# Performance work log

Measured on AMD Instinct MI355X. Metric: run time of the kernel, lower is better.

## Reference

```python
import jax, jax.numpy as jnp
import numpy as np

B, S, D, INNER = 4, 2048, 1024, 64  # batch, seq_len, input_size, cfg.inner_dim


def setup_inputs() -> dict:
    key = jax.random.key(0)
    ks = jax.random.split(key, 5)
    sequence_outputs = jax.random.normal(ks[0], (B, S, D), jnp.float32)
    W = jax.random.normal(ks[1], (INNER * 4, D), jnp.float32) * 0.02
    b = jnp.zeros((INNER * 4,), jnp.float32)
    similarity = jax.random.normal(ks[2], (B, S, S, 1), jnp.float32)
    input_labels = jax.random.randint(ks[3], (B, S, S), 0, 2)
    masks = jax.random.randint(ks[4], (B, S, S), 0, 2)
    return {"sequence_outputs": sequence_outputs, "W": W, "b": b,
            "similarity": similarity, "input_labels": input_labels, "masks": masks}


def _sincos(seq_len, dim):
    # RoPE with base 15 (pos_type=1 in the original code)
    pos = jnp.arange(seq_len, dtype=jnp.float32)[:, None]          # (S,1)
    inv = 15.0 ** (-2.0 * jnp.arange(dim // 2, dtype=jnp.float32) / dim)
    ang = pos * inv                                                # (S, dim/2)
    # interleaved [sin0,cos0,sin1,cos1,...] -> repeat_interleave(2) of odd/even slices
    sin = jnp.repeat(jnp.sin(ang), 2, axis=-1)                     # (S, dim)
    cos = jnp.repeat(jnp.cos(ang), 2, axis=-1)                     # (S, dim)
    return sin[None, :, None, :], cos[None, :, None, :]            # (1,S,1,dim)


def _rope(x, sin, cos):
    # x: (B,S,H,dim); rotate-half with interleaved pairs
    x2 = jnp.stack([-x[..., 1::2], x[..., ::2]], axis=-1).reshape(x.shape)
    return x * cos + x2 * sin


def reference(sequence_outputs, W, b, similarity, input_labels, masks):
    # dense: (B,S,D) -> (B,S,4*INNER); split into 2 chunks of 2*INNER, stacked on dim -2
    out = sequence_outputs @ W.T + b                               # (B,S,4I)
    out = out.reshape(B, S, 2, 2 * INNER)                          # (B,S,h=2,2I)
    qw, kw = out[..., :INNER], out[..., INNER:]                    # (B,S,2,I) each

    sin, cos = _sincos(S, INNER)
    qw = _rope(qw, sin, cos)
    kw = _rope(kw, sin, cos)

    pred_logits = jnp.einsum('bmhd,bnhd->bmnh', qw, kw) * similarity  # (B,S,S,2)

    # masked cross-entropy (CrossEntropyLoss with unit class weights, mean reduction)
    logp = jax.nn.log_softmax(pred_logits.reshape(-1, 2), axis=-1)
    lab = input_labels.reshape(-1)
    nll = -jnp.take_along_axis(logp, lab[:, None], axis=1)[:, 0]
    m = (masks.reshape(-1) == 1).astype(pred_logits.dtype)
    loss = jnp.sum(nll * m) / jnp.sum(m)
    return (loss, pred_logits)
```

## Files before the change

### kernel.cpp

```cpp
#include <hip/hip_runtime.h>
#include <hip/hip_bf16.h>
#include <math.h>

#define B_     4
#define S_     2048
#define D_     1024
#define INNER_ 64
#define M_     (B_ * S_)

typedef __attribute__((ext_vector_type(8))) short short8v;
typedef __attribute__((ext_vector_type(4))) float f32x4;

__device__ __forceinline__ unsigned short f32_to_bf16_rne(float f) {
    unsigned u = __float_as_uint(f);
    unsigned r = (u + 0x7FFFu + ((u >> 16) & 1u)) >> 16;
    return (unsigned short)r;
}
__device__ __forceinline__ float bf16_to_f32(unsigned short h) {
    return __uint_as_float((unsigned)h << 16);
}

__global__ __launch_bounds__(256)
void gemm1_rope_kernel(const float* __restrict__ seq, const float* __restrict__ W,
                       const float* __restrict__ bias,
                       unsigned short* __restrict__ qhl, unsigned short* __restrict__ khl) {
    const int bm = blockIdx.x;
    const int bn = blockIdx.y;
    __shared__ float As[16][65];
    __shared__ float Bs[16][65];
    __shared__ float s_inv[32];

    const int tid = threadIdx.x;
    if (tid < 32) s_inv[tid] = powf(15.0f, -(float)tid / 32.0f);

    const int tr = tid >> 4;
    const int tc = tid & 15;
    const int row0 = bm * 64, col0 = bn * 64;

    const int lr = tid >> 2;
    const int lc = (tid & 3) * 4;

    float acc[4][4] = {};

    for (int k0 = 0; k0 < D_; k0 += 16) {
        float4 av = *reinterpret_cast<const float4*>(&seq[(size_t)(row0 + lr) * D_ + k0 + lc]);
        float4 bv = *reinterpret_cast<const float4*>(&W  [(size_t)(col0 + lr) * D_ + k0 + lc]);
        As[lc + 0][lr] = av.x; As[lc + 1][lr] = av.y; As[lc + 2][lr] = av.z; As[lc + 3][lr] = av.w;
        Bs[lc + 0][lr] = bv.x; Bs[lc + 1][lr] = bv.y; Bs[lc + 2][lr] = bv.z; Bs[lc + 3][lr] = bv.w;
        __syncthreads();
#pragma unroll
        for (int kk = 0; kk < 16; ++kk) {
            float a[4], b[4];
#pragma unroll
            for (int i = 0; i < 4; ++i) a[i] = As[kk][tr * 4 + i];
#pragma unroll
            for (int j = 0; j < 4; ++j) b[j] = Bs[kk][tc * 4 + j];
#pragma unroll
            for (int i = 0; i < 4; ++i)
#pragma unroll
                for (int j = 0; j < 4; ++j)
                    acc[i][j] = fmaf(a[i], b[j], acc[i][j]);
        }
        __syncthreads();
    }

#pragma unroll
    for (int i = 0; i < 4; ++i) {
        const int m = row0 + tr * 4 + i;
        const int s = m & (S_ - 1);
#pragma unroll
        for (int jj = 0; jj < 4; jj += 2) {
            const int j = col0 + tc * 4 + jj;
            const float x0 = acc[i][jj]     + bias[j];
            const float x1 = acc[i][jj + 1] + bias[j + 1];
            const int h = j >> 7;
            const int c = j & 127;
            const int d = c & 63;
            const float inv = s_inv[d >> 1];
            const float ang = (float)s * inv;
            float sn, cs;
            __sincosf(ang, &sn, &cs);
            const float r0 = x0 * cs - x1 * sn;
            const float r1 = x1 * cs + x0 * sn;
            unsigned short* dst = (c < 64) ? qhl : khl;
            const unsigned short h0 = f32_to_bf16_rne(r0);
            const unsigned short h1 = f32_to_bf16_rne(r1);
            const unsigned short l0 = f32_to_bf16_rne(r0 - bf16_to_f32(h0));
            const unsigned short l1 = f32_to_bf16_rne(r1 - bf16_to_f32(h1));
            const size_t base = (size_t)m * 256 + (size_t)h * 128 + d;
            *reinterpret_cast<ushort2*>(&dst[base])      = make_ushort2(h0, h1);
            *reinterpret_cast<ushort2*>(&dst[base + 64]) = make_ushort2(l0, l1);
        }
    }
}

__global__ __launch_bounds__(256)
void qk_loss_kernel(const unsigned short* __restrict__ qhl,
                    const unsigned short* __restrict__ khl,
                    const float* __restrict__ sim, const int* __restrict__ labels,
                    const int* __restrict__ masks, float* __restrict__ logits,
                    double* __restrict__ accum) {
    const int bidx = blockIdx.x;
    const int bb = bidx >> 10;
    const int mt = (bidx >> 5) & 31;
    const int nt = bidx & 31;

    __shared__ __align__(16) unsigned short Ks[64][264];

    const int tid  = threadIdx.x;
    const int w    = tid >> 6;
    const int lane = tid & 63;
    const int lrow = lane & 15;
    const int lkg  = lane >> 4;

    {
        const unsigned short* kbase = khl + ((size_t)bb * S_ + (size_t)nt * 64) * 256;
#pragma unroll
        for (int it = 0; it < 8; ++it) {
            const int f = it * 256 + tid;
            const int r = f >> 5;
            const int ch = f & 31;
            *reinterpret_cast<uint4*>(reinterpret_cast<char*>(&Ks[0][0]) + r * 528 + ch * 16) =
                *reinterpret_cast<const uint4*>(kbase + (size_t)r * 256 + ch * 8);
        }
    }

    short8v qf[2][2][2];
    {
        const int mrow = mt * 64 + w * 16 + lrow;
        const unsigned short* qrow = qhl + ((size_t)bb * S_ + mrow) * 256;
#pragma unroll
        for (int h = 0; h < 2; ++h)
#pragma unroll
            for (int p = 0; p < 2; ++p)
#pragma unroll
                for (int s = 0; s < 2; ++s)
                    qf[h][p][s] = *reinterpret_cast<const short8v*>(
                        qrow + h * 128 + p * 64 + s * 32 + lkg * 8);
    }
    __syncthreads();

    f32x4 acc[2][4];
#pragma unroll
    for (int h = 0; h < 2; ++h)
#pragma unroll
        for (int cg = 0; cg < 4; ++cg)
            acc[h][cg] = (f32x4){0.f, 0.f, 0.f, 0.f};

#pragma unroll
    for (int h = 0; h < 2; ++h) {
#pragma unroll
        for (int cg = 0; cg < 4; ++cg) {
#pragma unroll
            for (int s = 0; s < 2; ++s) {
                const char* krow = reinterpret_cast<const char*>(&Ks[0][0]) +
                                   (cg * 16 + lrow) * 528 +
                                   h * 256 + s * 64 + lkg * 16;
                const short8v kh = *reinterpret_cast<const short8v*>(krow);
                const short8v kl = *reinterpret_cast<const short8v*>(krow + 128);
                acc[h][cg] = __builtin_amdgcn_mfma_f32_16x16x32_bf16(qf[h][0][s], kh, acc[h][cg], 0, 0, 0);
                acc[h][cg] = __builtin_amdgcn_mfma_f32_16x16x32_bf16(qf[h][0][s], kl, acc[h][cg], 0, 0, 0);
                acc[h][cg] = __builtin_amdgcn_mfma_f32_16x16x32_bf16(qf[h][1][s], kh, acc[h][cg], 0, 0, 0);
            }
        }
    }

    float lsum = 0.f, msum = 0.f;
#pragma unroll
    for (int cg = 0; cg < 4; ++cg) {
        const int n = nt * 64 + cg * 16 + lrow;
#pragma unroll
        for (int r = 0; r < 4; ++r) {
            const int m = mt * 64 + w * 16 + lkg * 4 + r;
            const size_t cell = ((size_t)bb * S_ + m) * S_ + n;
            const float sv = sim[cell];
            const float l0 = acc[0][cg][r] * sv;
            const float l1 = acc[1][cg][r] * sv;
            *reinterpret_cast<float2*>(&logits[cell * 2]) = make_float2(l0, l1);
            const int lab = labels[cell];
            const float mk = (masks[cell] == 1) ? 1.0f : 0.0f;
            const float mx = fmaxf(l0, l1);
            const float mn = fminf(l0, l1);
            const float lse = mx + log1pf(expf(mn - mx));
            const float nll = lse - (lab ? l1 : l0);
            lsum += nll * mk;
            msum += mk;
        }
    }

#pragma unroll
    for (int off = 32; off > 0; off >>= 1) {
        lsum += __shfl_down(lsum, off);
        msum += __shfl_down(msum, off);
    }
    __shared__ double wred[8];
    if (lane == 0) {
        wred[w]     = (double)lsum;
        wred[4 + w] = (double)msum;
    }
    __syncthreads();
    if (tid == 0) {
        atomicAdd(&accum[0], wred[0] + wred[1] + wred[2] + wred[3]);
        atomicAdd(&accum[1], wred[4] + wred[5] + wred[6] + wred[7]);
    }
}

__global__ void finalize_kernel(const double* __restrict__ accum, float* __restrict__ out) {
    out[0] = (float)(accum[0] / accum[1]);
}

extern "C" void kernel_launch(void* const* d_in, const int* in_sizes, int n_in,
                              void* d_out, int out_size, void* d_ws, size_t ws_size,
                              hipStream_t stream) {
    const float* seq    = (const float*)d_in[0];
    const float* W      = (const float*)d_in[1];
    const float* bias   = (const float*)d_in[2];
    const float* sim    = (const float*)d_in[3];
    const int*   labels = (const int*)d_in[4];
    const int*   masks  = (const int*)d_in[5];
    float* out = (float*)d_out;

    double* accum = (double*)d_ws;
    unsigned short* qhl = (unsigned short*)((char*)d_ws + 256);
    unsigned short* khl = qhl + (size_t)M_ * 256;

    hipMemsetAsync(d_ws, 0, 16, stream);

    dim3 gA(M_ / 64, 4);
    gemm1_rope_kernel<<<gA, 256, 0, stream>>>(seq, W, bias, qhl, khl);

    qk_loss_kernel<<<4096, 256, 0, stream>>>(qhl, khl, sim, labels, masks,
                                             out + 1, accum);

    finalize_kernel<<<1, 1, 0, stream>>>(accum, out);
}
```

Measured before the change: 498.8 us.

## Move projection GEMM to split-bf16 MFMA and split loss into separate kernel

```diff
diff --git a/kernel.cpp b/kernel.cpp
--- a/kernel.cpp
+++ b/kernel.cpp
@@ -5,7 +5,6 @@
 #define B_     4
 #define S_     2048
 #define D_     1024
-#define INNER_ 64
 #define M_     (B_ * S_)
 
 typedef __attribute__((ext_vector_type(8))) short short8v;
@@ -13,130 +12,148 @@
 
 __device__ __forceinline__ unsigned short f32_to_bf16_rne(float f) {
     unsigned u = __float_as_uint(f);
-    unsigned r = (u + 0x7FFFu + ((u >> 16) & 1u)) >> 16;
-    return (unsigned short)r;
+    return (unsigned short)((u + 0x7FFFu + ((u >> 16) & 1u)) >> 16);
 }
 __device__ __forceinline__ float bf16_to_f32(unsigned short h) {
     return __uint_as_float((unsigned)h << 16);
 }
 
-__global__ __launch_bounds__(256)
-void gemm1_rope_kernel(const float* __restrict__ seq, const float* __restrict__ W,
+__global__ __launch_bounds__(512)
+void gemm1_rope_kernel(const float* __restrict__ seq,
+                       const float* __restrict__ W,
                        const float* __restrict__ bias,
                        unsigned short* __restrict__ qhl, unsigned short* __restrict__ khl) {
     const int bm = blockIdx.x;
-    const int bn = blockIdx.y;
-    __shared__ float As[16][65];
-    __shared__ float Bs[16][65];
+    const int tid = threadIdx.x;
+    const int w = tid >> 6, lane = tid & 63;
+    const int lrow = lane & 15, lkg = lane >> 4;
+    const int wm = (w & 1) * 16;
+    const int jq = w >> 1;
+    const int m0 = bm * 32;
+
+    __shared__ __align__(16) unsigned short Sh[32][40], Sl[32][40];
+    __shared__ __align__(16) unsigned short Wth[256][40], Wtl[256][40];
     __shared__ float s_inv[32];
 
-    const int tid = threadIdx.x;
-    if (tid < 32) s_inv[tid] = powf(15.0f, -(float)tid / 32.0f);
-
-    const int tr = tid >> 4;
-    const int tc = tid & 15;
-    const int row0 = bm * 64, col0 = bn * 64;
-
-    const int lr = tid >> 2;
-    const int lc = (tid & 3) * 4;
-
-    float acc[4][4] = {};
-
-    for (int k0 = 0; k0 < D_; k0 += 16) {
-        float4 av = *reinterpret_cast<const float4*>(&seq[(size_t)(row0 + lr) * D_ + k0 + lc]);
-        float4 bv = *reinterpret_cast<const float4*>(&W  [(size_t)(col0 + lr) * D_ + k0 + lc]);
-        As[lc + 0][lr] = av.x; As[lc + 1][lr] = av.y; As[lc + 2][lr] = av.z; As[lc + 3][lr] = av.w;
-        Bs[lc + 0][lr] = bv.x; Bs[lc + 1][lr] = bv.y; Bs[lc + 2][lr] = bv.z; Bs[lc + 3][lr] = bv.w;
+    if (tid < 32) s_inv[tid] = (float)pow(15.0, -(double)tid / 32.0);
+
+    f32x4 acc[4];
+#pragma unroll
+    for (int i = 0; i < 4; ++i) acc[i] = (f32x4){0.f, 0.f, 0.f, 0.f};
+
+    const int srow = tid >> 3, scol = (tid & 7) * 4;
+
+    for (int k0 = 0; k0 < D_; k0 += 32) {
+        if (tid < 256) {
+            const float4 v = *reinterpret_cast<const float4*>(
+                seq + (size_t)(m0 + srow) * D_ + k0 + scol);
+            const unsigned short h0 = f32_to_bf16_rne(v.x), h1 = f32_to_bf16_rne(v.y),
+                                 h2 = f32_to_bf16_rne(v.z), h3 = f32_to_bf16_rne(v.w);
+            *reinterpret_cast<ushort4*>(&Sh[srow][scol]) = make_ushort4(h0, h1, h2, h3);
+            *reinterpret_cast<ushort4*>(&Sl[srow][scol]) =
+                make_ushort4(f32_to_bf16_rne(v.x - bf16_to_f32(h0)),
+                             f32_to_bf16_rne(v.y - bf16_to_f32(h1)),
+                             f32_to_bf16_rne(v.z - bf16_to_f32(h2)),
+                             f32_to_bf16_rne(v.w - bf16_to_f32(h3)));
+        }
+#pragma unroll
+        for (int p = 0; p < 4; ++p) {
+            const int c = tid + p * 512;
+            const int j = c >> 3;
+            const int kk = (c & 7) * 4;
+            const float4 v = *reinterpret_cast<const float4*>(
+                W + (size_t)j * D_ + k0 + kk);
+            const unsigned short h0 = f32_to_bf16_rne(v.x), h1 = f32_to_bf16_rne(v.y),
+                                 h2 = f32_to_bf16_rne(v.z), h3 = f32_to_bf16_rne(v.w);
+            *reinterpret_cast<ushort4*>(&Wth[j][kk]) = make_ushort4(h0, h1, h2, h3);
+            *reinterpret_cast<ushort4*>(&Wtl[j][kk]) =
+                make_ushort4(f32_to_bf16_rne(v.x - bf16_to_f32(h0)),
+                             f32_to_bf16_rne(v.y - bf16_to_f32(h1)),
+                             f32_to_bf16_rne(v.z - bf16_to_f32(h2)),
+                             f32_to_bf16_rne(v.w - bf16_to_f32(h3)));
+        }
         __syncthreads();
-#pragma unroll
-        for (int kk = 0; kk < 16; ++kk) {
-            float a[4], b[4];
-#pragma unroll
-            for (int i = 0; i < 4; ++i) a[i] = As[kk][tr * 4 + i];
-#pragma unroll
-            for (int j = 0; j < 4; ++j) b[j] = Bs[kk][tc * 4 + j];
-#pragma unroll
-            for (int i = 0; i < 4; ++i)
-#pragma unroll
-                for (int j = 0; j < 4; ++j)
-                    acc[i][j] = fmaf(a[i], b[j], acc[i][j]);
+
+        const short8v sh = *reinterpret_cast<const short8v*>(&Sh[wm + lrow][lkg * 8]);
+        const short8v sl = *reinterpret_cast<const short8v*>(&Sl[wm + lrow][lkg * 8]);
+#pragma unroll
+        for (int cg = 0; cg < 4; ++cg) {
+            const int jr = jq * 64 + cg * 16 + lrow;
+            const short8v wh = *reinterpret_cast<const short8v*>(&Wth[jr][lkg * 8]);
+            const short8v wl = *reinterpret_cast<const short8v*>(&Wtl[jr][lkg * 8]);
+            acc[cg] = __builtin_amdgcn_mfma_f32_16x16x32_bf16(wh, sh, acc[cg], 0, 0, 0);
+            acc[cg] = __builtin_amdgcn_mfma_f32_16x16x32_bf16(wh, sl, acc[cg], 0, 0, 0);
+            acc[cg] = __builtin_amdgcn_mfma_f32_16x16x32_bf16(wl, sh, acc[cg], 0, 0, 0);
         }
         __syncthreads();
     }
 
-#pragma unroll
-    for (int i = 0; i < 4; ++i) {
-        const int m = row0 + tr * 4 + i;
-        const int s = m & (S_ - 1);
-#pragma unroll
-        for (int jj = 0; jj < 4; jj += 2) {
-            const int j = col0 + tc * 4 + jj;
-            const float x0 = acc[i][jj]     + bias[j];
-            const float x1 = acc[i][jj + 1] + bias[j + 1];
-            const int h = j >> 7;
-            const int c = j & 127;
-            const int d = c & 63;
-            const float inv = s_inv[d >> 1];
-            const float ang = (float)s * inv;
-            float sn, cs;
-            __sincosf(ang, &sn, &cs);
-            const float r0 = x0 * cs - x1 * sn;
-            const float r1 = x1 * cs + x0 * sn;
-            unsigned short* dst = (c < 64) ? qhl : khl;
-            const unsigned short h0 = f32_to_bf16_rne(r0);
-            const unsigned short h1 = f32_to_bf16_rne(r1);
-            const unsigned short l0 = f32_to_bf16_rne(r0 - bf16_to_f32(h0));
-            const unsigned short l1 = f32_to_bf16_rne(r1 - bf16_to_f32(h1));
-            const size_t base = (size_t)m * 256 + (size_t)h * 128 + d;
-            *reinterpret_cast<ushort2*>(&dst[base])      = make_ushort2(h0, h1);
-            *reinterpret_cast<ushort2*>(&dst[base + 64]) = make_ushort2(l0, l1);
-        }
+    const int m = m0 + wm + lrow;
+    const int s = m & (S_ - 1);
+#pragma unroll
+    for (int cg = 0; cg < 4; ++cg) {
+        const int j0 = jq * 64 + cg * 16 + lkg * 4;
+        const float4 bv = *reinterpret_cast<const float4*>(bias + j0);
+        const float x0 = acc[cg][0] + bv.x, x1 = acc[cg][1] + bv.y;
+        const float x2 = acc[cg][2] + bv.z, x3 = acc[cg][3] + bv.w;
+        const int h = j0 >> 7;
+        const int c = j0 & 127;
+        const int d0 = c & 63;
+        float sn0, cs0, sn1, cs1;
+        __sincosf((float)s * s_inv[d0 >> 1],       &sn0, &cs0);
+        __sincosf((float)s * s_inv[(d0 >> 1) + 1], &sn1, &cs1);
+        const float r0 = x0 * cs0 - x1 * sn0;
+        const float r1 = x1 * cs0 + x0 * sn0;
+        const float r2 = x2 * cs1 - x3 * sn1;
+        const float r3 = x3 * cs1 + x2 * sn1;
+        const unsigned short a0 = f32_to_bf16_rne(r0), a1 = f32_to_bf16_rne(r1),
+                             a2 = f32_to_bf16_rne(r2), a3 = f32_to_bf16_rne(r3);
+        unsigned short* dst = (c < 64) ? qhl : khl;
+        const size_t base = (size_t)m * 256 + (size_t)h * 128 + d0;
+        *reinterpret_cast<ushort4*>(dst + base) = make_ushort4(a0, a1, a2, a3);
+        *reinterpret_cast<ushort4*>(dst + base + 64) =
+            make_ushort4(f32_to_bf16_rne(r0 - bf16_to_f32(a0)),
+                         f32_to_bf16_rne(r1 - bf16_to_f32(a1)),
+                         f32_to_bf16_rne(r2 - bf16_to_f32(a2)),
+                         f32_to_bf16_rne(r3 - bf16_to_f32(a3)));
     }
 }
 
 __global__ __launch_bounds__(256)
-void qk_loss_kernel(const unsigned short* __restrict__ qhl,
-                    const unsigned short* __restrict__ khl,
-                    const float* __restrict__ sim, const int* __restrict__ labels,
-                    const int* __restrict__ masks, float* __restrict__ logits,
-                    double* __restrict__ accum) {
+void qk_sim_kernel(const unsigned short* __restrict__ qhl,
+                   const unsigned short* __restrict__ khl,
+                   const float* __restrict__ sim,
+                   float* __restrict__ logits) {
     const int bidx = blockIdx.x;
-    const int bb = bidx >> 10;
-    const int mt = (bidx >> 5) & 31;
-    const int nt = bidx & 31;
-
+    const int bb = bidx >> 10, mt = (bidx >> 5) & 31, nt = bidx & 31;
     __shared__ __align__(16) unsigned short Ks[64][264];
 
-    const int tid  = threadIdx.x;
-    const int w    = tid >> 6;
-    const int lane = tid & 63;
-    const int lrow = lane & 15;
-    const int lkg  = lane >> 4;
+    const int tid = threadIdx.x, w = tid >> 6, lane = tid & 63;
+    const int lrow = lane & 15, lkg = lane >> 4;
 
     {
         const unsigned short* kbase = khl + ((size_t)bb * S_ + (size_t)nt * 64) * 256;
 #pragma unroll
         for (int it = 0; it < 8; ++it) {
             const int f = it * 256 + tid;
-            const int r = f >> 5;
-            const int ch = f & 31;
+            const int r = f >> 5, ch = f & 31;
             *reinterpret_cast<uint4*>(reinterpret_cast<char*>(&Ks[0][0]) + r * 528 + ch * 16) =
                 *reinterpret_cast<const uint4*>(kbase + (size_t)r * 256 + ch * 8);
         }
     }
 
+    const int mq = mt * 64 + w * 16 + lrow;
     short8v qf[2][2][2];
     {
-        const int mrow = mt * 64 + w * 16 + lrow;
-        const unsigned short* qrow = qhl + ((size_t)bb * S_ + mrow) * 256;
+        const unsigned short* qrow = qhl + ((size_t)bb * S_ + mq) * 256;
 #pragma unroll
         for (int h = 0; h < 2; ++h)
 #pragma unroll
             for (int p = 0; p < 2; ++p)
 #pragma unroll
-                for (int s = 0; s < 2; ++s)
-                    qf[h][p][s] = *reinterpret_cast<const short8v*>(
-                        qrow + h * 128 + p * 64 + s * 32 + lkg * 8);
+                for (int sx = 0; sx < 2; ++sx)
+                    qf[h][p][sx] = *reinterpret_cast<const short8v*>(
+                        qrow + h * 128 + p * 64 + sx * 32 + lkg * 8);
     }
     __syncthreads();
 
@@ -144,28 +161,23 @@
 #pragma unroll
     for (int h = 0; h < 2; ++h)
 #pragma unroll
+        for (int cg = 0; cg < 4; ++cg) acc[h][cg] = (f32x4){0.f, 0.f, 0.f, 0.f};
+
+#pragma unroll
+    for (int h = 0; h < 2; ++h)
+#pragma unroll
         for (int cg = 0; cg < 4; ++cg)
-            acc[h][cg] = (f32x4){0.f, 0.f, 0.f, 0.f};
-
-#pragma unroll
-    for (int h = 0; h < 2; ++h) {
-#pragma unroll
-        for (int cg = 0; cg < 4; ++cg) {
-#pragma unroll
-            for (int s = 0; s < 2; ++s) {
+#pragma unroll
+            for (int sx = 0; sx < 2; ++sx) {
                 const char* krow = reinterpret_cast<const char*>(&Ks[0][0]) +
-                                   (cg * 16 + lrow) * 528 +
-                                   h * 256 + s * 64 + lkg * 16;
+                                   (cg * 16 + lrow) * 528 + h * 256 + sx * 64 + lkg * 16;
                 const short8v kh = *reinterpret_cast<const short8v*>(krow);
                 const short8v kl = *reinterpret_cast<const short8v*>(krow + 128);
-                acc[h][cg] = __builtin_amdgcn_mfma_f32_16x16x32_bf16(qf[h][0][s], kh, acc[h][cg], 0, 0, 0);
-                acc[h][cg] = __builtin_amdgcn_mfma_f32_16x16x32_bf16(qf[h][0][s], kl, acc[h][cg], 0, 0, 0);
-                acc[h][cg] = __builtin_amdgcn_mfma_f32_16x16x32_bf16(qf[h][1][s], kh, acc[h][cg], 0, 0, 0);
+                acc[h][cg] = __builtin_amdgcn_mfma_f32_16x16x32_bf16(qf[h][0][sx], kh, acc[h][cg], 0, 0, 0);
+                acc[h][cg] = __builtin_amdgcn_mfma_f32_16x16x32_bf16(qf[h][0][sx], kl, acc[h][cg], 0, 0, 0);
+                acc[h][cg] = __builtin_amdgcn_mfma_f32_16x16x32_bf16(qf[h][1][sx], kh, acc[h][cg], 0, 0, 0);
             }
-        }
-    }
-
-    float lsum = 0.f, msum = 0.f;
+
 #pragma unroll
     for (int cg = 0; cg < 4; ++cg) {
         const int n = nt * 64 + cg * 16 + lrow;
@@ -174,32 +186,40 @@
             const int m = mt * 64 + w * 16 + lkg * 4 + r;
             const size_t cell = ((size_t)bb * S_ + m) * S_ + n;
             const float sv = sim[cell];
-            const float l0 = acc[0][cg][r] * sv;
-            const float l1 = acc[1][cg][r] * sv;
-            *reinterpret_cast<float2*>(&logits[cell * 2]) = make_float2(l0, l1);
-            const int lab = labels[cell];
-            const float mk = (masks[cell] == 1) ? 1.0f : 0.0f;
-            const float mx = fmaxf(l0, l1);
-            const float mn = fminf(l0, l1);
-            const float lse = mx + log1pf(expf(mn - mx));
-            const float nll = lse - (lab ? l1 : l0);
-            lsum += nll * mk;
-            msum += mk;
-        }
-    }
-
+            logits[cell * 2]     = acc[0][cg][r] * sv;
+            logits[cell * 2 + 1] = acc[1][cg][r] * sv;
+        }
+    }
+}
+
+__global__ __launch_bounds__(256)
+void loss_kernel(const float* __restrict__ logits, const int* __restrict__ labels,
+                 const int* __restrict__ masks, double* __restrict__ accum) {
+    const size_t NCELL = (size_t)B_ * S_ * S_;
+    const size_t stride = (size_t)gridDim.x * blockDim.x;
+    float lsum = 0.f, msum = 0.f;
+    for (size_t c = (size_t)blockIdx.x * blockDim.x + threadIdx.x; c < NCELL; c += stride) {
+        const float l0 = logits[c * 2];
+        const float l1 = logits[c * 2 + 1];
+        const int lab = labels[c];
+        const int mk  = masks[c];
+        const float mx = fmaxf(l0, l1), mn = fminf(l0, l1);
+        const float lse = mx + log1pf(expf(mn - mx));
+        const float nll = lse - (lab ? l1 : l0);
+        const float mf = (mk == 1) ? 1.0f : 0.0f;
+        lsum += nll * mf;
+        msum += mf;
+    }
 #pragma unroll
     for (int off = 32; off > 0; off >>= 1) {
         lsum += __shfl_down(lsum, off);
         msum += __shfl_down(msum, off);
     }
     __shared__ double wred[8];
-    if (lane == 0) {
-        wred[w]     = (double)lsum;
-        wred[4 + w] = (double)msum;
-    }
+    const int w = threadIdx.x >> 6;
+    if ((threadIdx.x & 63) == 0) { wred[w] = (double)lsum; wred[4 + w] = (double)msum; }
     __syncthreads();
-    if (tid == 0) {
+    if (threadIdx.x == 0) {
         atomicAdd(&accum[0], wred[0] + wred[1] + wred[2] + wred[3]);
         atomicAdd(&accum[1], wred[4] + wred[5] + wred[6] + wred[7]);
     }
@@ -218,19 +238,16 @@
     const float* sim    = (const float*)d_in[3];
     const int*   labels = (const int*)d_in[4];
     const int*   masks  = (const int*)d_in[5];
-    float* out = (float*)d_out;
+    float* out    = (float*)d_out;
+    float* logits = out + 1;
 
     double* accum = (double*)d_ws;
     unsigned short* qhl = (unsigned short*)((char*)d_ws + 256);
     unsigned short* khl = qhl + (size_t)M_ * 256;
 
-    hipMemsetAsync(d_ws, 0, 16, stream);
-
-    dim3 gA(M_ / 64, 4);
-    gemm1_rope_kernel<<<gA, 256, 0, stream>>>(seq, W, bias, qhl, khl);
-
-    qk_loss_kernel<<<4096, 256, 0, stream>>>(qhl, khl, sim, labels, masks,
-                                             out + 1, accum);
-
+    hipMemsetAsync(accum, 0, 16, stream);
+    gemm1_rope_kernel<<<256, 512, 0, stream>>>(seq, W, bias, qhl, khl);
+    qk_sim_kernel<<<4096, 256, 0, stream>>>(qhl, khl, sim, logits);
+    loss_kernel<<<2048, 256, 0, stream>>>(logits, labels, masks, accum);
     finalize_kernel<<<1, 1, 0, stream>>>(accum, out);
 }
```

Result: faster. 417.1 us (-16.4%).
